# Kernel tuning notes

Measured on AMD Instinct MI355X. Metric: run time of the kernel, lower is better.

The kernel has to match this reference:

```python
import jax, jax.numpy as jnp
import numpy as np

HEADS = 8
DIM_HEAD = 64
IMG_SIZE = 32
KERNEL = 5
DILATION = 1
SEQ_LEN = 1280
IMG_SEQ_LEN = IMG_SIZE * IMG_SIZE  # 1024
TEXT_LEN = SEQ_LEN - IMG_SEQ_LEN   # 256


def _unfold(t, k, pad, dil, pad_value=0.0):
    # t: (b, c, H, W) -> (b, c, H*W, k*k), matching torch F.unfold ordering (c major)
    b, c, H, W = t.shape
    tp = jnp.pad(t, ((0, 0), (0, 0), (pad, pad), (pad, pad)), constant_values=pad_value)
    off = jnp.arange(k) * dil
    ys = jnp.arange(H)[:, None] + off[None, :]  # (H, k)
    xs = jnp.arange(W)[:, None] + off[None, :]  # (W, k)
    p = tp[:, :, ys[:, None, :, None], xs[None, :, None, :]]  # (b, c, H, W, k, k)
    return p.reshape(b, c, H * W, k * k)


def setup_inputs() -> dict:
    key = jax.random.key(0)
    k0, k1, k2 = jax.random.split(key, 3)
    b, n, dim = 4, SEQ_LEN, 512
    inner = HEADS * DIM_HEAD
    x = jax.random.normal(k0, (b, n, dim), dtype=jnp.float32)
    mask = jnp.ones((b, TEXT_LEN), dtype=bool)
    W_qkv = jax.random.normal(k1, (dim, 3 * inner), dtype=jnp.float32) * 0.02
    W_out = jax.random.normal(k2, (inner, dim), dtype=jnp.float32) * 0.02
    b_out = jnp.zeros((dim,), dtype=jnp.float32)
    return {"x": x, "mask": mask, "W_qkv": W_qkv, "W_out": W_out, "b_out": b_out}


def reference(x, mask, W_qkv, W_out, b_out):
    # t2i branch of SparseConvCausalAttention.forward
    b, n, dim = x.shape
    h, d = HEADS, DIM_HEAD
    scale = d ** -0.5
    neg = -jnp.finfo(x.dtype).max
    eff_k = (KERNEL - 1) * DILATION + 1
    pad = eff_k // 2

    qkv = x @ W_qkv  # (b, n, 3*h*d); n == SEQ_LEN so F.pad is a no-op
    qkv = qkv.reshape(b, n, 3, h, d).transpose(2, 0, 3, 1, 4).reshape(3, b * h, n, d)
    q, k, v = qkv[0] * scale, qkv[1], qkv[2]

    q_text, q_img = q[:, :TEXT_LEN], q[:, TEXT_LEN:]
    k_text, k_img = k[:, :TEXT_LEN], k[:, TEXT_LEN:]
    v_text, v_img = v[:, :TEXT_LEN], v[:, TEXT_LEN:]

    # --- text -> text causal attention ---
    dots_text = jnp.einsum('bid,bjd->bij', q_text, k_text)  # (bh, T, T)
    causal_t = jnp.triu(jnp.ones((TEXT_LEN, TEXT_LEN), bool), 1)
    pad_mask = jnp.repeat(mask, h, axis=0)[:, None, :]  # (bh, 1, T)
    dots_text = jnp.where(causal_t[None], neg, dots_text)
    dots_text = jnp.where(~pad_mask, neg, dots_text)
    attn_text = jax.nn.softmax(dots_text, axis=-1)
    out_text = jnp.einsum('bij,bjd->bid', attn_text, v_text)

    # --- image local-window (unfold) keys/values ---
    k_im = k_img.transpose(0, 2, 1).reshape(b * h, d, IMG_SIZE, IMG_SIZE)
    v_im = v_img.transpose(0, 2, 1).reshape(b * h, d, IMG_SIZE, IMG_SIZE)
    kk = KERNEL * KERNEL
    k_patch = _unfold(k_im, KERNEL, pad, DILATION).transpose(0, 2, 3, 1)  # (bh, I, kk, d)
    v_patch = _unfold(v_im, KERNEL, pad, DILATION).transpose(0, 2, 3, 1)

    dots_image = jnp.einsum('bid,bijd->bij', q_img, k_patch)       # (bh, I, kk)
    dots_i2t = jnp.einsum('bid,bjd->bij', q_img, k_text)           # (bh, I, T)

    # local causal mask via unfolded position indices (out-of-bounds -> IMG_SEQ_LEN)
    idx_img = jnp.arange(IMG_SEQ_LEN, dtype=jnp.float32).reshape(1, 1, IMG_SIZE, IMG_SIZE)
    k_idx = _unfold(idx_img, KERNEL, pad, DILATION, pad_value=float(IMG_SEQ_LEN))
    k_idx = k_idx.reshape(IMG_SEQ_LEN, kk)  # (I, kk)
    q_idx = jnp.arange(IMG_SEQ_LEN, dtype=jnp.float32)[:, None]
    causal_img = q_idx < k_idx  # (I, kk)

    full_mask = jnp.concatenate(
        (jnp.broadcast_to(~pad_mask, (b * h, IMG_SEQ_LEN, TEXT_LEN)),
         jnp.broadcast_to(causal_img[None], (b * h, IMG_SEQ_LEN, kk))), axis=-1)
    dots = jnp.concatenate((dots_i2t, dots_image), axis=-1)
    dots = jnp.where(full_mask, neg, dots)
    attn = jax.nn.softmax(dots, axis=-1)
    attn_i2t, attn_ii = attn[..., :TEXT_LEN], attn[..., TEXT_LEN:]

    out_img = (jnp.einsum('bij,bijd->bid', attn_ii, v_patch)
               + jnp.einsum('bij,bjd->bid', attn_i2t, v_text))

    out = jnp.concatenate((out_text, out_img), axis=1)  # (bh, n, d)
    out = out.reshape(b, h, n, d).transpose(0, 2, 1, 3).reshape(b, n, h * d)
    out = out @ W_out + b_out
    return out[:, :n]
```

## Files before the change

### kernel.cpp

```cpp
#include <hip/hip_runtime.h>
#include <math.h>

#define BATCH   4
#define NSEQ    1280
#define DIM     512
#define HEADS   8
#define DHEAD   64
#define TEXTLEN 256
#define IMGLEN  1024
#define BH      (BATCH*HEADS)

typedef __bf16 bf16x8 __attribute__((ext_vector_type(8)));
typedef __bf16 bf16x4 __attribute__((ext_vector_type(4)));
typedef float  f32x4  __attribute__((ext_vector_type(4)));
typedef unsigned short u16x4 __attribute__((ext_vector_type(4)));
typedef unsigned short u16x8 __attribute__((ext_vector_type(8)));

__device__ __forceinline__ unsigned short f2bf(float f) {
  unsigned int u = __float_as_uint(f);
  u += 0x7FFFu + ((u >> 16) & 1u);
  return (unsigned short)(u >> 16);
}

template<int MODE>
__global__ __launch_bounds__(256)
void mfma_gemm(const unsigned short* __restrict__ A,
               const unsigned short* __restrict__ BT,
               unsigned short* __restrict__ qb, unsigned short* __restrict__ kb,
               unsigned short* __restrict__ vb, unsigned short* __restrict__ vt,
               float* __restrict__ outb, const float* __restrict__ bias) {
  __shared__ __align__(16) unsigned short As[128*64];
  __shared__ __align__(16) unsigned short Bs[128*64];
  const int tid  = threadIdx.x;
  const int lane = tid & 63, w = tid >> 6;
  const int wm = w >> 1, wn = w & 1;
  const int lr = lane & 15, lg = lane >> 4;
  const int bx = blockIdx.x, by = blockIdx.y;

  f32x4 acc[4][4] = {};

  for (int kt = 0; kt < 512; kt += 64) {
    __syncthreads();
#pragma unroll
    for (int u = 0; u < 4; ++u) {
      const int idx = tid + u*256;
      const int row = idx >> 3, pq = idx & 7;
      const int sc  = ((pq ^ (row & 7)) << 3);
      const unsigned short* ga = A  + (size_t)(by*128 + row)*512 + kt + sc;
      const unsigned short* gb = BT + (size_t)(bx*128 + row)*512 + kt + sc;
      unsigned short* la = As + (((u << 8) + (w << 6)) << 3);
      unsigned short* lb = Bs + (((u << 8) + (w << 6)) << 3);
      __builtin_amdgcn_global_load_lds(
          (const __attribute__((address_space(1))) void*)ga,
          (__attribute__((address_space(3))) void*)la, 16, 0, 0);
      __builtin_amdgcn_global_load_lds(
          (const __attribute__((address_space(1))) void*)gb,
          (__attribute__((address_space(3))) void*)lb, 16, 0, 0);
    }
    __syncthreads();

#pragma unroll
    for (int kk = 0; kk < 2; ++kk) {
      bf16x8 af[4], bfr[4];
#pragma unroll
      for (int mi = 0; mi < 4; ++mi) {
        const int row = wm*64 + mi*16 + lr;
        const int q   = kk*4 + lg;
        af[mi] = *(const bf16x8*)&As[row*64 + ((q ^ (row & 7)) << 3)];
      }
#pragma unroll
      for (int ni = 0; ni < 4; ++ni) {
        const int n = wn*64 + ni*16 + lr;
        const int q = kk*4 + lg;
        bfr[ni] = *(const bf16x8*)&Bs[n*64 + ((q ^ (n & 7)) << 3)];
      }
#pragma unroll
      for (int mi = 0; mi < 4; ++mi)
#pragma unroll
        for (int ni = 0; ni < 4; ++ni)
          acc[mi][ni] = __builtin_amdgcn_mfma_f32_16x16x32_bf16(
              af[mi], bfr[ni], acc[mi][ni], 0, 0, 0);
    }
  }

  if (MODE == 0) {
    const int t  = bx >> 2, bxl = bx & 3;
    const int hh = bxl*2 + wn;
    const int bb = by / 10;
    const int nb = (by - bb*10) * 128;
    const float s = (t == 0) ? 0.125f : 1.0f;
    const size_t bh64 = (size_t)(bb*HEADS + hh);
    if (t != 2) {
      unsigned short* dst = (t == 0) ? qb : kb;
      unsigned short* base = dst + (bh64*NSEQ + nb)*DHEAD;
#pragma unroll
      for (int mi = 0; mi < 4; ++mi)
#pragma unroll
        for (int ni = 0; ni < 4; ++ni)
#pragma unroll
          for (int r = 0; r < 4; ++r) {
            const int rl = wm*64 + mi*16 + lg*4 + r;
            base[(size_t)rl*DHEAD + ni*16 + lr] = f2bf(acc[mi][ni][r] * s);
          }
    } else if (nb < 256) {
      unsigned short* vtb = vt + bh64*64*TEXTLEN;
#pragma unroll
      for (int mi = 0; mi < 4; ++mi)
#pragma unroll
        for (int ni = 0; ni < 4; ++ni)
#pragma unroll
          for (int r = 0; r < 4; ++r) {
            const int key = nb + wm*64 + mi*16 + lg*4 + r;
            const int d   = ni*16 + lr;
            const int p   = key >> 5, w16 = (key >> 4) & 1;
            const int g2  = (key >> 2) & 3, r2 = key & 3;
            vtb[(size_t)d*256 + p*32 + g2*8 + w16*4 + r2] = f2bf(acc[mi][ni][r]);
          }
    } else {
      unsigned short* base = vb + (bh64*NSEQ + nb)*DHEAD;
#pragma unroll
      for (int mi = 0; mi < 4; ++mi)
#pragma unroll
        for (int ni = 0; ni < 4; ++ni)
#pragma unroll
          for (int r = 0; r < 4; ++r) {
            const int rl = wm*64 + mi*16 + lg*4 + r;
            const int d  = ni*16 + lr;
            const int jd = d >> 4, gg = (d >> 2) & 3, rr = d & 3;
            const int pos = ((jd >> 1) << 5) + (gg << 3) + ((jd & 1) << 2) + rr;
            base[(size_t)rl*DHEAD + pos] = f2bf(acc[mi][ni][r]);
          }
    }
  } else {
#pragma unroll
    for (int mi = 0; mi < 4; ++mi)
#pragma unroll
      for (int ni = 0; ni < 4; ++ni)
#pragma unroll
        for (int r = 0; r < 4; ++r) {
          const int gr = by*128 + wm*64 + mi*16 + lg*4 + r;
          const int gc = bx*128 + wn*64 + ni*16 + lr;
          outb[(size_t)gr*DIM + gc] = acc[mi][ni][r] + bias[gc];
        }
  }
}

__global__ __launch_bounds__(256)
void convert_bf16(const float* __restrict__ in, unsigned short* __restrict__ out,
                  int n) {
  const int i = (blockIdx.x*256 + threadIdx.x)*8;
  if (i < n) {
    const float4 a = *(const float4*)(in + i);
    const float4 b = *(const float4*)(in + i + 4);
    u16x8 pk;
    pk[0]=f2bf(a.x); pk[1]=f2bf(a.y); pk[2]=f2bf(a.z); pk[3]=f2bf(a.w);
    pk[4]=f2bf(b.x); pk[5]=f2bf(b.y); pk[6]=f2bf(b.z); pk[7]=f2bf(b.w);
    *(u16x8*)(out + i) = pk;
  }
}

__global__ __launch_bounds__(256)
void transpose_bf16(const float* __restrict__ in, unsigned short* __restrict__ out,
                    int K, int N) {
  __shared__ float t[64][65];
  const int k0 = blockIdx.y*64, n0 = blockIdx.x*64;
  const int tx = threadIdx.x & 15, ty = threadIdx.x >> 4;
#pragma unroll
  for (int rr = 0; rr < 4; ++rr) {
    const int k = ty + rr*16;
    const float4 v = *(const float4*)(in + (size_t)(k0 + k)*N + n0 + tx*4);
    t[k][tx*4+0] = v.x; t[k][tx*4+1] = v.y; t[k][tx*4+2] = v.z; t[k][tx*4+3] = v.w;
  }
  __syncthreads();
#pragma unroll
  for (int rr = 0; rr < 4; ++rr) {
    const int n = ty + rr*16;
    u16x4 pk;
#pragma unroll
    for (int j = 0; j < 4; ++j) pk[j] = f2bf(t[tx*4+j][n]);
    *(u16x4*)(out + (size_t)(n0 + n)*K + k0 + tx*4) = pk;
  }
}

__global__ __launch_bounds__(256)
void attn_fused(const unsigned short* __restrict__ qv,
                const unsigned short* __restrict__ kv,
                const unsigned short* __restrict__ vv,
                const unsigned short* __restrict__ vt,
                unsigned short* __restrict__ ab) {
  __shared__ __align__(16) unsigned short Ks[256*64];
  const int idx  = blockIdx.x;
  const int xcd  = idx & 7, slot = idx >> 3;
  const int bh   = (slot / 20) * 8 + xcd;
  const int sub  = slot - (slot / 20) * 20;
  const bool img = sub < 16;
  const int qblk = img ? sub : (sub - 16);
  const int bb = bh >> 3, hh = bh & 7;
  const int tid = threadIdx.x;
  const int w = tid >> 6;
  const int lane = tid & 63;
  const int lr = lane & 15, g = lane >> 4;
  const int rs = lr & 7;
  const int qi = qblk*64 + w*16 + lr;
  const int qrow = img ? (TEXTLEN + qi) : qi;

  {
    const unsigned short* kgb = kv + (size_t)bh*NSEQ*DHEAD;
#pragma unroll
    for (int u = 0; u < 8; ++u) {
      const int ci = tid + u*256;
      const int row = ci >> 3, cq = ci & 7;
      const unsigned short* gsrc = kgb + row*64 + ((cq ^ (row & 7)) << 3);
      unsigned short* ldst = Ks + (((u << 8) + (w << 6)) << 3);
      __builtin_amdgcn_global_load_lds(
          (const __attribute__((address_space(1))) void*)gsrc,
          (__attribute__((address_space(3))) void*)ldst, 16, 0, 0);
    }
  }

  const unsigned short* qp = qv + ((size_t)bh*NSEQ + qrow)*DHEAD;
  const bf16x8 qf0 = *(const bf16x8*)(qp + g*8);
  const bf16x8 qf1 = *(const bf16x8*)(qp + 32 + g*8);

  const unsigned short* vbase = vt + (size_t)(bh*64 + lr)*256 + g*8;
  bf16x8 vbuf[2][4];
#pragma unroll
  for (int pp = 0; pp < 2; ++pp)
#pragma unroll
    for (int jd = 0; jd < 4; ++jd)
      vbuf[pp][jd] = *(const bf16x8*)(vbase + (size_t)jd*4096 + pp*32);

  __syncthreads();

  f32x4 s[8][2];
#pragma unroll
  for (int p = 0; p < 8; ++p) {
    const int r0 = p*32 + lr, r1 = r0 + 16;
    f32x4 a0 = {0.f,0.f,0.f,0.f}, a1 = {0.f,0.f,0.f,0.f};
    a0 = __builtin_amdgcn_mfma_f32_16x16x32_bf16(
        *(const bf16x8*)&Ks[r0*64 + ((g       ^ rs) << 3)], qf0, a0, 0,0,0);
    a0 = __builtin_amdgcn_mfma_f32_16x16x32_bf16(
        *(const bf16x8*)&Ks[r0*64 + (((4 + g) ^ rs) << 3)], qf1, a0, 0,0,0);
    a1 = __builtin_amdgcn_mfma_f32_16x16x32_bf16(
        *(const bf16x8*)&Ks[r1*64 + ((g       ^ rs) << 3)], qf0, a1, 0,0,0);
    a1 = __builtin_amdgcn_mfma_f32_16x16x32_bf16(
        *(const bf16x8*)&Ks[r1*64 + (((4 + g) ^ rs) << 3)], qf1, a1, 0,0,0);
    s[p][0] = a0; s[p][1] = a1;
  }
  if (!img) {
#pragma unroll
    for (int p = 0; p < 8; ++p)
#pragma unroll
      for (int t = 0; t < 2; ++t)
#pragma unroll
        for (int r = 0; r < 4; ++r)
          if (p*32 + t*16 + 4*g + r > qi) s[p][t][r] = -3.0e38f;
  }

  float M = -3.0e38f;
#pragma unroll
  for (int p = 0; p < 8; ++p)
#pragma unroll
    for (int t = 0; t < 2; ++t)
#pragma unroll
      for (int r = 0; r < 4; ++r) M = fmaxf(M, s[p][t][r]);
  M = fmaxf(M, __shfl_xor(M, 16));
  M = fmaxf(M, __shfl_xor(M, 32));

  f32x4 o[4] = {};
  float l = 0.f;
#pragma unroll
  for (int p = 0; p < 8; ++p) {
    bf16x8 pf;
#pragma unroll
    for (int t = 0; t < 2; ++t)
#pragma unroll
      for (int r = 0; r < 4; ++r) {
        const float wv = __expf(s[p][t][r] - M);
        l += wv;
        pf[t*4 + r] = (__bf16)wv;
      }
#pragma unroll
    for (int jd = 0; jd < 4; ++jd)
      o[jd] = __builtin_amdgcn_mfma_f32_16x16x32_bf16(vbuf[p & 1][jd], pf,
                                                      o[jd], 0, 0, 0);
    if (p + 2 < 8) {
#pragma unroll
      for (int jd = 0; jd < 4; ++jd)
        vbuf[p & 1][jd] = *(const bf16x8*)(vbase + (size_t)jd*4096 + (p + 2)*32);
    }
  }

  if (img) {
    float qd[16];
#pragma unroll
    for (int e = 0; e < 8; ++e) { qd[e] = (float)qf0[e]; qd[8+e] = (float)qf1[e]; }
    const int yy = qi >> 5, xx = qi & 31;
    const int NBY[13] = {-2,-2,-2,-2,-2,-1,-1,-1,-1,-1, 0, 0, 0};
    const int NBX[13] = {-2,-1, 0, 1, 2,-2,-1, 0, 1, 2,-2,-1, 0};
    float dnb[13];
#pragma unroll
    for (int nb = 0; nb < 13; ++nb) {
      const int ny = yy + NBY[nb], nx = xx + NBX[nb];
      const bool ok = (ny >= 0) && ((unsigned)nx < 32u);
      const int kidx = ok ? (ny*32 + nx) : qi;
      const unsigned short* kr = kv + ((size_t)bh*NSEQ + TEXTLEN + kidx)*DHEAD;
      const bf16x8 k0 = *(const bf16x8*)(kr + g*8);
      const bf16x8 k1 = *(const bf16x8*)(kr + 32 + g*8);
      float d = 0.f;
#pragma unroll
      for (int e = 0; e < 8; ++e) d += qd[e]*(float)k0[e] + qd[8+e]*(float)k1[e];
      d += __shfl_xor(d, 16);
      d += __shfl_xor(d, 32);
      dnb[nb] = ok ? d : -3.0e38f;
    }
    float tm = dnb[0];
#pragma unroll
    for (int nb = 1; nb < 13; ++nb) tm = fmaxf(tm, dnb[nb]);
    const float mn = fmaxf(M, tm);
    const float cf = __expf(M - mn);
    l *= cf;
#pragma unroll
    for (int jd = 0; jd < 4; ++jd)
#pragma unroll
      for (int r = 0; r < 4; ++r) o[jd][r] *= cf;
    float lacc = 0.f;
#pragma unroll
    for (int nb = 0; nb < 13; ++nb) {
      const int ny = yy + NBY[nb], nx = xx + NBX[nb];
      const bool ok = (ny >= 0) && ((unsigned)nx < 32u);
      const int kidx = ok ? (ny*32 + nx) : qi;
      const float wv = __expf(dnb[nb] - mn);
      lacc += wv;
      const unsigned short* vr = vv + ((size_t)bh*NSEQ + TEXTLEN + kidx)*DHEAD;
      const bf16x8 c0 = *(const bf16x8*)(vr + g*8);
      const bf16x8 c1 = *(const bf16x8*)(vr + 32 + g*8);
#pragma unroll
      for (int r = 0; r < 4; ++r) {
        o[0][r] += wv*(float)c0[r];
        o[1][r] += wv*(float)c0[4+r];
        o[2][r] += wv*(float)c1[r];
        o[3][r] += wv*(float)c1[4+r];
      }
    }
    if (g == 0) l += lacc;
  }

  float lf = l;
  lf += __shfl_xor(lf, 16);
  lf += __shfl_xor(lf, 32);
  const float inv = 1.f / lf;
  unsigned short* op = ab + ((size_t)(bb*NSEQ) + qrow)*DIM + hh*DHEAD;
#pragma unroll
  for (int jd = 0; jd < 4; ++jd) {
    u16x4 pk;
#pragma unroll
    for (int r = 0; r < 4; ++r) pk[r] = f2bf(o[jd][r]*inv);
    *(u16x4*)(op + jd*16 + g*4) = pk;
  }
}

extern "C" void kernel_launch(void* const* d_in, const int* in_sizes, int n_in,
                              void* d_out, int out_size, void* d_ws, size_t ws_size,
                              hipStream_t stream) {
  const float* x     = (const float*)d_in[0];
  const float* W_qkv = (const float*)d_in[2];
  const float* W_out = (const float*)d_in[3];
  const float* b_out = (const float*)d_in[4];
  float* out = (float*)d_out;

  unsigned short* w = (unsigned short*)d_ws;
  const size_t P = (size_t)BH*NSEQ*DHEAD;
  unsigned short* qb  = w;
  unsigned short* kb  = qb + P;
  unsigned short* vb  = kb + P;
  unsigned short* xb  = vb + P;
  unsigned short* ab  = xb;
  unsigned short* wtq = xb + P;
  unsigned short* wto = wtq + (size_t)1536*512;
  unsigned short* vtb = wto + (size_t)512*512;

  convert_bf16<<<(BATCH*NSEQ*DIM)/(256*8), 256, 0, stream>>>(x, xb, BATCH*NSEQ*DIM);
  transpose_bf16<<<dim3(24, 8), 256, 0, stream>>>(W_qkv, wtq, 512, 1536);
  transpose_bf16<<<dim3(8, 8), 256, 0, stream>>>(W_out, wto, 512, 512);

  mfma_gemm<0><<<dim3(12, 40), 256, 0, stream>>>(
      xb, wtq, qb, kb, vb, vtb, nullptr, nullptr);

  attn_fused<<<BH*16 + BH*4, 256, 0, stream>>>(qb, kb, vb, vtb, ab);

  mfma_gemm<1><<<dim3(4, 40), 256, 0, stream>>>(
      ab, wto, nullptr, nullptr, nullptr, nullptr, out, b_out);
}
```

Baseline: 75.92 us.

## Split fused attention into QK GEMM, PV GEMM and finalize kernels

Replaces the single fused attention kernel with three kernels. The first computes QK^T tiles and stores unnormalised exp probabilities plus partial row sums to global memory. The second does a tiled P·V GEMM into fp32. The third adds the 13-neighbour local image terms and normalises. Softmax skips max subtraction, which risks overflow for larger scores, and the change adds substantial intermediate global traffic and extra launches in exchange for regular GEMM tiling.

```diff
diff --git a/kernel.cpp b/kernel.cpp
--- a/kernel.cpp
+++ b/kernel.cpp
@@ -11,7 +11,6 @@
 #define BH      (BATCH*HEADS)
 
 typedef __bf16 bf16x8 __attribute__((ext_vector_type(8)));
-typedef __bf16 bf16x4 __attribute__((ext_vector_type(4)));
 typedef float  f32x4  __attribute__((ext_vector_type(4)));
 typedef unsigned short u16x4 __attribute__((ext_vector_type(4)));
 typedef unsigned short u16x8 __attribute__((ext_vector_type(8)));
@@ -110,11 +109,9 @@
         for (int ni = 0; ni < 4; ++ni)
 #pragma unroll
           for (int r = 0; r < 4; ++r) {
-            const int key = nb + wm*64 + mi*16 + lg*4 + r;
-            const int d   = ni*16 + lr;
-            const int p   = key >> 5, w16 = (key >> 4) & 1;
-            const int g2  = (key >> 2) & 3, r2 = key & 3;
-            vtb[(size_t)d*256 + p*32 + g2*8 + w16*4 + r2] = f2bf(acc[mi][ni][r]);
+            const int rl = wm*64 + mi*16 + lg*4 + r;
+            const int d  = ni*16 + lr;
+            vtb[(size_t)d*TEXTLEN + nb + rl] = f2bf(acc[mi][ni][r]);
           }
     } else {
       unsigned short* base = vb + (bh64*NSEQ + nb)*DHEAD;
@@ -125,10 +122,7 @@
 #pragma unroll
           for (int r = 0; r < 4; ++r) {
             const int rl = wm*64 + mi*16 + lg*4 + r;
-            const int d  = ni*16 + lr;
-            const int jd = d >> 4, gg = (d >> 2) & 3, rr = d & 3;
-            const int pos = ((jd >> 1) << 5) + (gg << 3) + ((jd & 1) << 2) + rr;
-            base[(size_t)rl*DHEAD + pos] = f2bf(acc[mi][ni][r]);
+            base[(size_t)rl*DHEAD + ni*16 + lr] = f2bf(acc[mi][ni][r]);
           }
     }
   } else {
@@ -183,181 +177,228 @@
 }
 
 __global__ __launch_bounds__(256)
-void attn_fused(const unsigned short* __restrict__ qv,
-                const unsigned short* __restrict__ kv,
-                const unsigned short* __restrict__ vv,
-                const unsigned short* __restrict__ vt,
-                unsigned short* __restrict__ ab) {
-  __shared__ __align__(16) unsigned short Ks[256*64];
-  const int idx  = blockIdx.x;
-  const int xcd  = idx & 7, slot = idx >> 3;
-  const int bh   = (slot / 20) * 8 + xcd;
-  const int sub  = slot - (slot / 20) * 20;
-  const bool img = sub < 16;
-  const int qblk = img ? sub : (sub - 16);
+void attn_qk(const unsigned short* __restrict__ qv,
+             const unsigned short* __restrict__ kv,
+             unsigned short* __restrict__ Pm, float* __restrict__ lpart) {
+  __shared__ __align__(16) unsigned short As[128*64];
+  __shared__ __align__(16) unsigned short Bs[128*64];
+  const int tid  = threadIdx.x;
+  const int lane = tid & 63, w = tid >> 6;
+  const int wm = w >> 1, wn = w & 1;
+  const int lr = lane & 15, lg = lane >> 4;
+  const int bx = blockIdx.x, by = blockIdx.y;
+  const int bh = by / 10, qt = by - bh*10;
+  const bool textq = qt >= 8;
+  const int qsrc  = textq ? (qt - 8)*128 : (TEXTLEN + qt*128);
+  const int prow0 = qt*128;
+  const int qg0   = (qt - 8)*128;
+
+  {
+    const unsigned short* ga0 = qv + ((size_t)bh*NSEQ + qsrc)*DHEAD;
+    const unsigned short* gb0 = kv + ((size_t)bh*NSEQ + bx*128)*DHEAD;
+#pragma unroll
+    for (int u = 0; u < 4; ++u) {
+      const int idx = tid + u*256;
+      const int row = idx >> 3, pq = idx & 7;
+      const int sc  = ((pq ^ (row & 7)) << 3);
+      unsigned short* la = As + (((u << 8) + (w << 6)) << 3);
+      unsigned short* lb = Bs + (((u << 8) + (w << 6)) << 3);
+      __builtin_amdgcn_global_load_lds(
+          (const __attribute__((address_space(1))) void*)(ga0 + (size_t)row*DHEAD + sc),
+          (__attribute__((address_space(3))) void*)la, 16, 0, 0);
+      __builtin_amdgcn_global_load_lds(
+          (const __attribute__((address_space(1))) void*)(gb0 + (size_t)row*DHEAD + sc),
+          (__attribute__((address_space(3))) void*)lb, 16, 0, 0);
+    }
+  }
+  __syncthreads();
+
+  f32x4 acc[4][4] = {};
+#pragma unroll
+  for (int kk = 0; kk < 2; ++kk) {
+    bf16x8 af[4], bfr[4];
+#pragma unroll
+    for (int mi = 0; mi < 4; ++mi) {
+      const int row = wm*64 + mi*16 + lr;
+      const int q   = kk*4 + lg;
+      af[mi] = *(const bf16x8*)&As[row*64 + ((q ^ (row & 7)) << 3)];
+    }
+#pragma unroll
+    for (int ni = 0; ni < 4; ++ni) {
+      const int n = wn*64 + ni*16 + lr;
+      const int q = kk*4 + lg;
+      bfr[ni] = *(const bf16x8*)&Bs[n*64 + ((q ^ (n & 7)) << 3)];
+    }
+#pragma unroll
+    for (int mi = 0; mi < 4; ++mi)
+#pragma unroll
+      for (int ni = 0; ni < 4; ++ni)
+        acc[mi][ni] = __builtin_amdgcn_mfma_f32_16x16x32_bf16(
+            af[mi], bfr[ni], acc[mi][ni], 0, 0, 0);
+  }
+
+  unsigned short* pbase = Pm + ((size_t)bh*NSEQ + prow0)*TEXTLEN;
+  float* lbase = lpart + ((size_t)bh*NSEQ + prow0)*4;
+#pragma unroll
+  for (int mi = 0; mi < 4; ++mi)
+#pragma unroll
+    for (int r = 0; r < 4; ++r) {
+      const int q_local = wm*64 + mi*16 + lg*4 + r;
+      float ps = 0.f;
+#pragma unroll
+      for (int ni = 0; ni < 4; ++ni) {
+        const int key = bx*128 + wn*64 + ni*16 + lr;
+        float wv = __expf(acc[mi][ni][r]);
+        if (textq && key > qg0 + q_local) wv = 0.f;
+        ps += wv;
+        pbase[(size_t)q_local*TEXTLEN + key] = f2bf(wv);
+      }
+      ps += __shfl_xor(ps, 1);
+      ps += __shfl_xor(ps, 2);
+      ps += __shfl_xor(ps, 4);
+      ps += __shfl_xor(ps, 8);
+      if (lr == 0) lbase[(size_t)q_local*4 + bx*2 + wn] = ps;
+    }
+}
+
+__global__ __launch_bounds__(256)
+void attn_pv(const unsigned short* __restrict__ Pm,
+             const unsigned short* __restrict__ vt,
+             float* __restrict__ Of) {
+  __shared__ __align__(16) unsigned short As[256*64];
+  __shared__ __align__(16) unsigned short Bs[64*64];
+  const int tid  = threadIdx.x;
+  const int lane = tid & 63, w = tid >> 6;
+  const int lr = lane & 15, lg = lane >> 4;
+  const int mt = blockIdx.x, bh = blockIdx.y;
+
+  f32x4 acc[4][4] = {};
+
+  for (int kt = 0; kt < TEXTLEN; kt += 64) {
+    __syncthreads();
+    {
+      const unsigned short* ga0 = Pm + ((size_t)bh*NSEQ + mt*256)*TEXTLEN + kt;
+      const unsigned short* gb0 = vt + ((size_t)bh*DHEAD)*TEXTLEN + kt;
+#pragma unroll
+      for (int u = 0; u < 8; ++u) {
+        const int idx = tid + u*256;
+        const int row = idx >> 3, pq = idx & 7;
+        const int sc  = ((pq ^ (row & 7)) << 3);
+        unsigned short* la = As + (((u << 8) + (w << 6)) << 3);
+        __builtin_amdgcn_global_load_lds(
+            (const __attribute__((address_space(1))) void*)(ga0 + (size_t)row*TEXTLEN + sc),
+            (__attribute__((address_space(3))) void*)la, 16, 0, 0);
+      }
+#pragma unroll
+      for (int u = 0; u < 2; ++u) {
+        const int idx = tid + u*256;
+        const int row = idx >> 3, pq = idx & 7;
+        const int sc  = ((pq ^ (row & 7)) << 3);
+        unsigned short* lb = Bs + (((u << 8) + (w << 6)) << 3);
+        __builtin_amdgcn_global_load_lds(
+            (const __attribute__((address_space(1))) void*)(gb0 + (size_t)row*TEXTLEN + sc),
+            (__attribute__((address_space(3))) void*)lb, 16, 0, 0);
+      }
+    }
+    __syncthreads();
+
+#pragma unroll
+    for (int kk = 0; kk < 2; ++kk) {
+      bf16x8 af[4], bfr[4];
+#pragma unroll
+      for (int mi = 0; mi < 4; ++mi) {
+        const int row = w*64 + mi*16 + lr;
+        const int q   = kk*4 + lg;
+        af[mi] = *(const bf16x8*)&As[row*64 + ((q ^ (row & 7)) << 3)];
+      }
+#pragma unroll
+      for (int ni = 0; ni < 4; ++ni) {
+        const int n = ni*16 + lr;
+        const int q = kk*4 + lg;
+        bfr[ni] = *(const bf16x8*)&Bs[n*64 + ((q ^ (n & 7)) << 3)];
+      }
+#pragma unroll
+      for (int mi = 0; mi < 4; ++mi)
+#pragma unroll
+        for (int ni = 0; ni < 4; ++ni)
+          acc[mi][ni] = __builtin_amdgcn_mfma_f32_16x16x32_bf16(
+              af[mi], bfr[ni], acc[mi][ni], 0, 0, 0);
+    }
+  }
+
+  float* obase = Of + ((size_t)bh*NSEQ + mt*256)*DHEAD;
+#pragma unroll
+  for (int mi = 0; mi < 4; ++mi)
+#pragma unroll
+    for (int ni = 0; ni < 4; ++ni)
+#pragma unroll
+      for (int r = 0; r < 4; ++r) {
+        const int row = w*64 + mi*16 + lg*4 + r;
+        obase[(size_t)row*DHEAD + ni*16 + lr] = acc[mi][ni][r];
+      }
+}
+
+__global__ __launch_bounds__(256)
+void attn_fin(const unsigned short* __restrict__ qv,
+              const unsigned short* __restrict__ kv,
+              const unsigned short* __restrict__ vb,
+              const float* __restrict__ Of, const float* __restrict__ lpart,
+              unsigned short* __restrict__ ab) {
+  const int blk = blockIdx.x;
+  const int bh = blk / 40, sub = blk - bh*40;
   const int bb = bh >> 3, hh = bh & 7;
-  const int tid = threadIdx.x;
-  const int w = tid >> 6;
-  const int lane = tid & 63;
-  const int lr = lane & 15, g = lane >> 4;
-  const int rs = lr & 7;
-  const int qi = qblk*64 + w*16 + lr;
-  const int qrow = img ? (TEXTLEN + qi) : qi;
-
+  const int gq = threadIdx.x >> 3;
+  const int s8 = threadIdx.x & 7;
+  const int prow = sub*32 + gq;
+  const bool img = prow < IMGLEN;
+  const int qrow = img ? (TEXTLEN + prow) : (prow - IMGLEN);
+
+  float o[8];
   {
-    const unsigned short* kgb = kv + (size_t)bh*NSEQ*DHEAD;
-#pragma unroll
-    for (int u = 0; u < 8; ++u) {
-      const int ci = tid + u*256;
-      const int row = ci >> 3, cq = ci & 7;
-      const unsigned short* gsrc = kgb + row*64 + ((cq ^ (row & 7)) << 3);
-      unsigned short* ldst = Ks + (((u << 8) + (w << 6)) << 3);
-      __builtin_amdgcn_global_load_lds(
-          (const __attribute__((address_space(1))) void*)gsrc,
-          (__attribute__((address_space(3))) void*)ldst, 16, 0, 0);
-    }
-  }
-
-  const unsigned short* qp = qv + ((size_t)bh*NSEQ + qrow)*DHEAD;
-  const bf16x8 qf0 = *(const bf16x8*)(qp + g*8);
-  const bf16x8 qf1 = *(const bf16x8*)(qp + 32 + g*8);
-
-  const unsigned short* vbase = vt + (size_t)(bh*64 + lr)*256 + g*8;
-  bf16x8 vbuf[2][4];
-#pragma unroll
-  for (int pp = 0; pp < 2; ++pp)
-#pragma unroll
-    for (int jd = 0; jd < 4; ++jd)
-      vbuf[pp][jd] = *(const bf16x8*)(vbase + (size_t)jd*4096 + pp*32);
-
-  __syncthreads();
-
-  f32x4 s[8][2];
-#pragma unroll
-  for (int p = 0; p < 8; ++p) {
-    const int r0 = p*32 + lr, r1 = r0 + 16;
-    f32x4 a0 = {0.f,0.f,0.f,0.f}, a1 = {0.f,0.f,0.f,0.f};
-    a0 = __builtin_amdgcn_mfma_f32_16x16x32_bf16(
-        *(const bf16x8*)&Ks[r0*64 + ((g       ^ rs) << 3)], qf0, a0, 0,0,0);
-    a0 = __builtin_amdgcn_mfma_f32_16x16x32_bf16(
-        *(const bf16x8*)&Ks[r0*64 + (((4 + g) ^ rs) << 3)], qf1, a0, 0,0,0);
-    a1 = __builtin_amdgcn_mfma_f32_16x16x32_bf16(
-        *(const bf16x8*)&Ks[r1*64 + ((g       ^ rs) << 3)], qf0, a1, 0,0,0);
-    a1 = __builtin_amdgcn_mfma_f32_16x16x32_bf16(
-        *(const bf16x8*)&Ks[r1*64 + (((4 + g) ^ rs) << 3)], qf1, a1, 0,0,0);
-    s[p][0] = a0; s[p][1] = a1;
-  }
-  if (!img) {
-#pragma unroll
-    for (int p = 0; p < 8; ++p)
-#pragma unroll
-      for (int t = 0; t < 2; ++t)
-#pragma unroll
-        for (int r = 0; r < 4; ++r)
-          if (p*32 + t*16 + 4*g + r > qi) s[p][t][r] = -3.0e38f;
-  }
-
-  float M = -3.0e38f;
-#pragma unroll
-  for (int p = 0; p < 8; ++p)
-#pragma unroll
-    for (int t = 0; t < 2; ++t)
-#pragma unroll
-      for (int r = 0; r < 4; ++r) M = fmaxf(M, s[p][t][r]);
-  M = fmaxf(M, __shfl_xor(M, 16));
-  M = fmaxf(M, __shfl_xor(M, 32));
-
-  f32x4 o[4] = {};
-  float l = 0.f;
-#pragma unroll
-  for (int p = 0; p < 8; ++p) {
-    bf16x8 pf;
-#pragma unroll
-    for (int t = 0; t < 2; ++t)
-#pragma unroll
-      for (int r = 0; r < 4; ++r) {
-        const float wv = __expf(s[p][t][r] - M);
-        l += wv;
-        pf[t*4 + r] = (__bf16)wv;
-      }
-#pragma unroll
-    for (int jd = 0; jd < 4; ++jd)
-      o[jd] = __builtin_amdgcn_mfma_f32_16x16x32_bf16(vbuf[p & 1][jd], pf,
-                                                      o[jd], 0, 0, 0);
-    if (p + 2 < 8) {
-#pragma unroll
-      for (int jd = 0; jd < 4; ++jd)
-        vbuf[p & 1][jd] = *(const bf16x8*)(vbase + (size_t)jd*4096 + (p + 2)*32);
-    }
+    const float4 a = *(const float4*)(Of + ((size_t)bh*NSEQ + prow)*DHEAD + s8*8);
+    const float4 b = *(const float4*)(Of + ((size_t)bh*NSEQ + prow)*DHEAD + s8*8 + 4);
+    o[0]=a.x; o[1]=a.y; o[2]=a.z; o[3]=a.w; o[4]=b.x; o[5]=b.y; o[6]=b.z; o[7]=b.w;
+  }
+  float l;
+  {
+    const float4 lp = *(const float4*)(lpart + ((size_t)bh*NSEQ + prow)*4);
+    l = lp.x + lp.y + lp.z + lp.w;
   }
 
   if (img) {
-    float qd[16];
-#pragma unroll
-    for (int e = 0; e < 8; ++e) { qd[e] = (float)qf0[e]; qd[8+e] = (float)qf1[e]; }
-    const int yy = qi >> 5, xx = qi & 31;
-    const int NBY[13] = {-2,-2,-2,-2,-2,-1,-1,-1,-1,-1, 0, 0, 0};
-    const int NBX[13] = {-2,-1, 0, 1, 2,-2,-1, 0, 1, 2,-2,-1, 0};
-    float dnb[13];
-#pragma unroll
+    float qd[8];
+    {
+      const bf16x8 q8 = *(const bf16x8*)(qv + ((size_t)bh*NSEQ + qrow)*DHEAD + s8*8);
+#pragma unroll
+      for (int e = 0; e < 8; ++e) qd[e] = (float)q8[e];
+    }
+    const int yy = prow >> 5, xx = prow & 31;
     for (int nb = 0; nb < 13; ++nb) {
-      const int ny = yy + NBY[nb], nx = xx + NBX[nb];
+      const int q5 = nb / 5;
+      const int ny = yy + q5 - 2;
+      const int nx = xx + (nb - q5*5) - 2;
       const bool ok = (ny >= 0) && ((unsigned)nx < 32u);
-      const int kidx = ok ? (ny*32 + nx) : qi;
-      const unsigned short* kr = kv + ((size_t)bh*NSEQ + TEXTLEN + kidx)*DHEAD;
-      const bf16x8 k0 = *(const bf16x8*)(kr + g*8);
-      const bf16x8 k1 = *(const bf16x8*)(kr + 32 + g*8);
+      const int kidx = ok ? (ny*32 + nx) : prow;
+      const bf16x8 k8 = *(const bf16x8*)(kv + ((size_t)bh*NSEQ + TEXTLEN + kidx)*DHEAD + s8*8);
       float d = 0.f;
 #pragma unroll
-      for (int e = 0; e < 8; ++e) d += qd[e]*(float)k0[e] + qd[8+e]*(float)k1[e];
-      d += __shfl_xor(d, 16);
-      d += __shfl_xor(d, 32);
-      dnb[nb] = ok ? d : -3.0e38f;
-    }
-    float tm = dnb[0];
-#pragma unroll
-    for (int nb = 1; nb < 13; ++nb) tm = fmaxf(tm, dnb[nb]);
-    const float mn = fmaxf(M, tm);
-    const float cf = __expf(M - mn);
-    l *= cf;
-#pragma unroll
-    for (int jd = 0; jd < 4; ++jd)
-#pragma unroll
-      for (int r = 0; r < 4; ++r) o[jd][r] *= cf;
-    float lacc = 0.f;
-#pragma unroll
-    for (int nb = 0; nb < 13; ++nb) {
-      const int ny = yy + NBY[nb], nx = xx + NBX[nb];
-      const bool ok = (ny >= 0) && ((unsigned)nx < 32u);
-      const int kidx = ok ? (ny*32 + nx) : qi;
-      const float wv = __expf(dnb[nb] - mn);
-      lacc += wv;
-      const unsigned short* vr = vv + ((size_t)bh*NSEQ + TEXTLEN + kidx)*DHEAD;
-      const bf16x8 c0 = *(const bf16x8*)(vr + g*8);
-      const bf16x8 c1 = *(const bf16x8*)(vr + 32 + g*8);
-#pragma unroll
-      for (int r = 0; r < 4; ++r) {
-        o[0][r] += wv*(float)c0[r];
-        o[1][r] += wv*(float)c0[4+r];
-        o[2][r] += wv*(float)c1[r];
-        o[3][r] += wv*(float)c1[4+r];
-      }
-    }
-    if (g == 0) l += lacc;
-  }
-
-  float lf = l;
-  lf += __shfl_xor(lf, 16);
-  lf += __shfl_xor(lf, 32);
-  const float inv = 1.f / lf;
-  unsigned short* op = ab + ((size_t)(bb*NSEQ) + qrow)*DIM + hh*DHEAD;
-#pragma unroll
-  for (int jd = 0; jd < 4; ++jd) {
-    u16x4 pk;
-#pragma unroll
-    for (int r = 0; r < 4; ++r) pk[r] = f2bf(o[jd][r]*inv);
-    *(u16x4*)(op + jd*16 + g*4) = pk;
-  }
+      for (int e = 0; e < 8; ++e) d += qd[e]*(float)k8[e];
+      d += __shfl_xor(d, 1);
+      d += __shfl_xor(d, 2);
+      d += __shfl_xor(d, 4);
+      const float wv = ok ? __expf(d) : 0.f;
+      l += wv;
+      const bf16x8 v8 = *(const bf16x8*)(vb + ((size_t)bh*NSEQ + TEXTLEN + kidx)*DHEAD + s8*8);
+#pragma unroll
+      for (int e = 0; e < 8; ++e) o[e] += wv*(float)v8[e];
+    }
+  }
+
+  const float inv = 1.f / l;
+  u16x8 pk;
+#pragma unroll
+  for (int e = 0; e < 8; ++e) pk[e] = f2bf(o[e]*inv);
+  *(u16x8*)(ab + ((size_t)(bb*NSEQ) + qrow)*DIM + hh*DHEAD + s8*8) = pk;
 }
 
 extern "C" void kernel_launch(void* const* d_in, const int* in_sizes, int n_in,
@@ -379,6 +420,9 @@
   unsigned short* wtq = xb + P;
   unsigned short* wto = wtq + (size_t)1536*512;
   unsigned short* vtb = wto + (size_t)512*512;
+  unsigned short* Pm  = vtb + (size_t)BH*DHEAD*TEXTLEN;
+  float* Of    = (float*)(Pm + (size_t)BH*NSEQ*TEXTLEN);
+  float* lpart = Of + (size_t)BH*NSEQ*DHEAD;
 
   convert_bf16<<<(BATCH*NSEQ*DIM)/(256*8), 256, 0, stream>>>(x, xb, BATCH*NSEQ*DIM);
   transpose_bf16<<<dim3(24, 8), 256, 0, stream>>>(W_qkv, wtq, 512, 1536);
@@ -387,7 +431,9 @@
   mfma_gemm<0><<<dim3(12, 40), 256, 0, stream>>>(
       xb, wtq, qb, kb, vb, vtb, nullptr, nullptr);
 
-  attn_fused<<<BH*16 + BH*4, 256, 0, stream>>>(qb, kb, vb, vtb, ab);
+  attn_qk<<<dim3(2, 320), 256, 0, stream>>>(qb, kb, Pm, lpart);
+  attn_pv<<<dim3(5, 32), 256, 0, stream>>>(Pm, vtb, Of);
+  attn_fin<<<1280, 256, 0, stream>>>(qb, kb, vb, Of, lpart, ab);
 
   mfma_gemm<1><<<dim3(4, 40), 256, 0, stream>>>(
       ab, wto, nullptr, nullptr, nullptr, nullptr, out, b_out);
```

Result: no change. 76.02 us (+0.1%).
